# Performance work log

Hardware: AMD Instinct MI355X
Metric: run time of the kernel (lower is better)

## Reference

```python
import jax, jax.numpy as jnp
import numpy as np

B, D, E, TOP_K = 16384, 2048, 8, 2


def setup_inputs() -> dict:
    key = jax.random.key(0)
    ks = jax.random.split(key, 5)
    scale = 1.0 / np.sqrt(D)
    x = jax.random.normal(ks[0], (B, D), dtype=jnp.float32)
    # expert Linear(D, D) weights/biases, stacked over experts
    expert_w = jax.random.uniform(ks[1], (E, D, D), minval=-scale, maxval=scale, dtype=jnp.float32)
    expert_b = jax.random.uniform(ks[2], (E, D), minval=-scale, maxval=scale, dtype=jnp.float32)
    # gate Linear(D, E)
    gate_w = jax.random.uniform(ks[3], (D, E), minval=-scale, maxval=scale, dtype=jnp.float32)
    gate_b = jax.random.uniform(ks[4], (E,), minval=-scale, maxval=scale, dtype=jnp.float32)
    return {"x": x, "expert_w": expert_w, "expert_b": expert_b, "gate_w": gate_w, "gate_b": gate_b}


def reference(x, expert_w, expert_b, gate_w, gate_b):
    # gate logits: (B, E)
    logits = x @ gate_w + gate_b
    topk_logits, topk_idx = jax.lax.top_k(logits, TOP_K)          # (B, K)
    topk_weights = jax.nn.softmax(topk_logits, axis=-1)           # (B, K)
    # dense: compute every expert for every token (faithful to original)
    expert_outputs = jax.nn.relu(
        jnp.einsum("bd,edf->bef", x, expert_w) + expert_b[None, :, :]
    )                                                             # (B, E, D); dropout is identity in eval mode
    # gather the top-k experts per token
    selected = jnp.take_along_axis(expert_outputs, topk_idx[:, :, None], axis=1)  # (B, K, D)
    out = jnp.sum(selected * topk_weights[:, :, None], axis=1)    # (B, D)
    return out
```

## Files before the change

kernel.cpp:

```cpp
#include <hip/hip_runtime.h>
#include <hip/hip_bf16.h>
#include <math.h>

#define NB 16384
#define DD 2048
#define NE 8
#define TM 128
#define TN 128
#define BK 64
#define NKT (DD / BK)
#define MT_PER_PASS (NB / TM + NE)
#define NT_TILES (DD / TN)
#define GEMM_GRID (MT_PER_PASS * NT_TILES)

typedef float f32x4 __attribute__((ext_vector_type(4)));
typedef short bf16x8 __attribute__((ext_vector_type(8)));

__device__ __forceinline__ short f2bf(float f) {
  union { float f; unsigned u; } v; v.f = f;
  unsigned r = (v.u + 0x7FFFu + ((v.u >> 16) & 1u)) >> 16;
  return (short)r;
}

__device__ __forceinline__ void gload16(const void* g, void* l) {
  __builtin_amdgcn_global_load_lds((const __attribute__((address_space(1))) void*)g,
                                   (__attribute__((address_space(3))) void*)l,
                                   16, 0, 0);
}

__global__ void conv_wT(const float* __restrict__ w, short* __restrict__ wt) {
  __shared__ float tile[64][68];
  int bid = blockIdx.x;
  int e = bid >> 10;
  int tt = bid & 1023;
  int d0 = (tt >> 5) << 6;
  int f0 = (tt & 31) << 6;
  const float* we = w + (size_t)e * DD * DD;
  int t = threadIdx.x;
  int col = (t & 15) << 2;
#pragma unroll
  for (int p = 0; p < 4; ++p) {
    int dl = (t >> 4) + p * 16;
    f32x4 v = *(const f32x4*)(we + (size_t)(d0 + dl) * DD + f0 + col);
    *(f32x4*)&tile[dl][col] = v;
  }
  __syncthreads();
  int fl = t >> 2;
  int ds = (t & 3) << 4;
  short tmp[16];
#pragma unroll
  for (int j = 0; j < 16; ++j) tmp[j] = f2bf(tile[ds + j][fl]);
  short* dst = wt + (size_t)e * DD * DD + (size_t)(f0 + fl) * DD + d0 + ds;
  *(bf16x8*)dst = *(const bf16x8*)tmp;
  *(bf16x8*)(dst + 8) = *(const bf16x8*)(tmp + 8);
}

__global__ void gate_conv(const float* __restrict__ x, const float* __restrict__ gw,
                          const float* __restrict__ gb, short* __restrict__ xb,
                          int* __restrict__ ridx, float* __restrict__ rw) {
  int wid = threadIdx.x >> 6;
  int lane = threadIdx.x & 63;
  int b = blockIdx.x * 4 + wid;
  const float* xr = x + (size_t)b * DD;
  short* xbr = xb + (size_t)b * DD;
  double acc[8];
#pragma unroll
  for (int e = 0; e < 8; ++e) acc[e] = 0.0;
#pragma unroll
  for (int it = 0; it < 4; ++it) {
    int d8 = (it * 64 + lane) * 8;
    f32x4 a = *(const f32x4*)(xr + d8);
    f32x4 c = *(const f32x4*)(xr + d8 + 4);
    bf16x8 o;
    o[0] = f2bf(a[0]); o[1] = f2bf(a[1]); o[2] = f2bf(a[2]); o[3] = f2bf(a[3]);
    o[4] = f2bf(c[0]); o[5] = f2bf(c[1]); o[6] = f2bf(c[2]); o[7] = f2bf(c[3]);
    *(bf16x8*)(xbr + d8) = o;
#pragma unroll
    for (int j = 0; j < 8; ++j) {
      float xv = (j < 4) ? a[j] : c[j - 4];
      double xd = (double)xv;
      f32x4 g0 = *(const f32x4*)(gw + (size_t)(d8 + j) * 8);
      f32x4 g1 = *(const f32x4*)(gw + (size_t)(d8 + j) * 8 + 4);
      acc[0] += xd * g0[0]; acc[1] += xd * g0[1];
      acc[2] += xd * g0[2]; acc[3] += xd * g0[3];
      acc[4] += xd * g1[0]; acc[5] += xd * g1[1];
      acc[6] += xd * g1[2]; acc[7] += xd * g1[3];
    }
  }
#pragma unroll
  for (int off = 32; off > 0; off >>= 1) {
#pragma unroll
    for (int e = 0; e < 8; ++e) acc[e] += __shfl_down(acc[e], off);
  }
  if (lane == 0) {
    double l[8];
#pragma unroll
    for (int e = 0; e < 8; ++e) l[e] = acc[e] + (double)gb[e];
    int i0 = 0;
#pragma unroll
    for (int e = 1; e < 8; ++e) if (l[e] > l[i0]) i0 = e;
    int i1 = (i0 == 0) ? 1 : 0;
#pragma unroll
    for (int e = 0; e < 8; ++e) if (e != i0 && l[e] > l[i1]) i1 = e;
    double z = exp(l[i1] - l[i0]);
    float w0 = (float)(1.0 / (1.0 + z));
    float w1 = (float)(z / (1.0 + z));
    ridx[2 * b] = i0; ridx[2 * b + 1] = i1;
    rw[2 * b] = w0;   rw[2 * b + 1] = w1;
  }
}

__global__ void hist_tok(const int* __restrict__ ridx, int* __restrict__ partials) {
  __shared__ int h[16];
  int t = threadIdx.x;
  if (t < 16) h[t] = 0;
  __syncthreads();
  int t0 = blockIdx.x * 512;
  for (int i = t; i < 512; i += 256) {
    int tok = t0 + i;
    atomicAdd(&h[ridx[2 * tok]], 1);
    atomicAdd(&h[8 + ridx[2 * tok + 1]], 1);
  }
  __syncthreads();
  if (t < 16) partials[blockIdx.x * 16 + t] = h[t];
}

__global__ void scan_small(const int* __restrict__ partials, int* __restrict__ base,
                           int* __restrict__ cnts, int* __restrict__ offs) {
  __shared__ int c[16], o[16];
  int j = threadIdx.x;
  if (j < 16) {
    int s = 0;
    for (int b = 0; b < 32; ++b) s += partials[b * 16 + j];
    c[j] = s; cnts[j] = s;
  }
  __syncthreads();
  if (j < 2) {
    int a = 0;
    for (int e = 0; e < 8; ++e) { o[j * 8 + e] = a; a += c[j * 8 + e]; }
  }
  __syncthreads();
  if (j < 16) {
    int r = o[j];
    offs[j] = o[j];
    for (int b = 0; b < 32; ++b) { base[b * 16 + j] = r; r += partials[b * 16 + j]; }
  }
}

__global__ void scatter_tok(const int* __restrict__ ridx, const float* __restrict__ rw,
                            const int* __restrict__ base,
                            int* __restrict__ lists0, float* __restrict__ elw0,
                            int* __restrict__ lists1, float* __restrict__ elw1) {
  __shared__ int h[16];
  int t = threadIdx.x;
  if (t < 16) h[t] = 0;
  __syncthreads();
  int t0 = blockIdx.x * 512;
  const int* bb = base + blockIdx.x * 16;
  for (int i = t; i < 512; i += 256) {
    int tok = t0 + i;
    int e0 = ridx[2 * tok], e1 = ridx[2 * tok + 1];
    int r0 = atomicAdd(&h[e0], 1);
    int r1 = atomicAdd(&h[8 + e1], 1);
    int p0 = bb[e0] + r0;
    int p1 = bb[8 + e1] + r1;
    lists0[p0] = tok; elw0[p0] = rw[2 * tok];
    lists1[p1] = tok; elw1[p1] = rw[2 * tok + 1];
  }
}

template <int ADD>
__global__ __launch_bounds__(256, 4)
void moe_gemm(const short* __restrict__ xb, const short* __restrict__ wt,
              const float* __restrict__ eb, const int* __restrict__ cnts,
              const int* __restrict__ offs, const int* __restrict__ lists,
              const float* __restrict__ elw, float* __restrict__ out) {
  __shared__ short As[TM * BK];
  __shared__ short Bs[TN * BK];

  int bid = blockIdx.x;
  int xcd = bid & 7;
  int j = bid >> 3;
  int mt = xcd * 17 + (j >> 4);
  int nt = j & 15;

  int e = 0, cnt = 0;
  for (; e < NE; ++e) {
    cnt = cnts[e];
    int te = (cnt + TM - 1) >> 7;
    if (mt < te) break;
    mt -= te;
  }
  if (e >= NE) return;

  int m0 = mt * TM;
  int n0 = nt * TN;
  int off_e = offs[e];
  int tid = threadIdx.x;
  int lane = tid & 63, wid = tid >> 6;
  int wr = wid >> 1, wc = wid & 1;

  int trow = tid >> 3;
  int scol = ((tid & 7) ^ (trow & 7)) << 3;
  int tok[4];
#pragma unroll
  for (int l = 0; l < 4; ++l) {
    int gr = m0 + l * 32 + trow;
    tok[l] = lists[off_e + ((gr < cnt) ? gr : (cnt - 1))];
  }
  const short* bbase = wt + ((size_t)e * DD + (size_t)(n0 + trow)) * DD + scol;

  int lane15 = lane & 15;
  int csw0 = (((lane >> 4)    ) ^ (lane & 7)) << 3;
  int csw1 = (((lane >> 4) + 4) ^ (lane & 7)) << 3;
  int arow = (wr * 64 + lane15) * 64;
  int brow = (wc * 64 + lane15) * 64;

  f32x4 acc[4][4];
#pragma unroll
  for (int i = 0; i < 4; ++i)
#pragma unroll
    for (int j2 = 0; j2 < 4; ++j2) acc[i][j2] = (f32x4){0.f, 0.f, 0.f, 0.f};

#pragma unroll 1
  for (int kt = 0; kt < NKT; ++kt) {
    int ko = kt * BK + scol;
#pragma unroll
    for (int l = 0; l < 4; ++l) {
      gload16(xb + ((size_t)tok[l] << 11) + ko, &As[l * 2048 + tid * 8]);
      gload16(bbase + (size_t)(l * 32) * DD + kt * BK, &Bs[l * 2048 + tid * 8]);
    }
    __syncthreads();
    bf16x8 bfr[4][2];
#pragma unroll
    for (int j2 = 0; j2 < 4; ++j2) {
      int br = brow + j2 * 16 * 64;
      bfr[j2][0] = *(const bf16x8*)&Bs[br + csw0];
      bfr[j2][1] = *(const bf16x8*)&Bs[br + csw1];
    }
#pragma unroll
    for (int i = 0; i < 4; ++i) {
      int ar = arow + i * 16 * 64;
      bf16x8 a0 = *(const bf16x8*)&As[ar + csw0];
      bf16x8 a1 = *(const bf16x8*)&As[ar + csw1];
#pragma unroll
      for (int j2 = 0; j2 < 4; ++j2) {
        acc[i][j2] = __builtin_amdgcn_mfma_f32_16x16x32_bf16(a0, bfr[j2][0], acc[i][j2], 0, 0, 0);
        acc[i][j2] = __builtin_amdgcn_mfma_f32_16x16x32_bf16(a1, bfr[j2][1], acc[i][j2], 0, 0, 0);
      }
    }
    __syncthreads();
  }

  int r0 = (lane >> 4) << 2;
#pragma unroll
  for (int i = 0; i < 4; ++i) {
    int mloc = wr * 64 + i * 16 + r0;
#pragma unroll
    for (int r = 0; r < 4; ++r) {
      int gr = m0 + mloc + r;
      if (gr >= cnt) continue;
      int tokr = lists[off_e + gr];
      float wgt = elw[off_e + gr];
      float* orow = out + (size_t)tokr * DD;
#pragma unroll
      for (int j2 = 0; j2 < 4; ++j2) {
        int n = n0 + wc * 64 + j2 * 16 + lane15;
        float v = acc[i][j2][r] + eb[e * DD + n];
        v = fmaxf(v, 0.f) * wgt;
        if (ADD) v += __builtin_nontemporal_load(&orow[n]);
        __builtin_nontemporal_store(v, &orow[n]);
      }
    }
  }
}

extern "C" void kernel_launch(void* const* d_in, const int* in_sizes, int n_in,
                              void* d_out, int out_size, void* d_ws, size_t ws_size,
                              hipStream_t stream) {
  const float* x   = (const float*)d_in[0];
  const float* ewt = (const float*)d_in[1];
  const float* eb  = (const float*)d_in[2];
  const float* gw  = (const float*)d_in[3];
  const float* gb  = (const float*)d_in[4];
  float* out = (float*)d_out;

  char* ws = (char*)d_ws;
  short* xb      = (short*)(ws);
  short* wt      = (short*)(ws + 67108864);
  int*   ridx    = (int*)  (ws + 134217728);
  float* rw      = (float*)(ws + 134348800);
  int*   lists0  = (int*)  (ws + 134479872);
  float* elw0    = (float*)(ws + 134545408);
  int*   lists1  = (int*)  (ws + 134610944);
  float* elw1    = (float*)(ws + 134676480);
  int*   partials= (int*)  (ws + 134742016);
  int*   base    = (int*)  (ws + 134744064);
  int*   cnts    = (int*)  (ws + 134746112);
  int*   offs    = (int*)  (ws + 134746176);

  conv_wT<<<NE * 32 * 32, 256, 0, stream>>>(ewt, wt);
  gate_conv<<<NB / 4, 256, 0, stream>>>(x, gw, gb, xb, ridx, rw);
  hist_tok<<<32, 256, 0, stream>>>(ridx, partials);
  scan_small<<<1, 64, 0, stream>>>(partials, base, cnts, offs);
  scatter_tok<<<32, 256, 0, stream>>>(ridx, rw, base, lists0, elw0, lists1, elw1);
  moe_gemm<0><<<GEMM_GRID, 256, 0, stream>>>(xb, wt, eb, cnts,     offs,     lists0, elw0, out);
  moe_gemm<1><<<GEMM_GRID, 256, 0, stream>>>(xb, wt, eb, cnts + 8, offs + 8, lists1, elw1, out);
}
```

Measured before the change: 540.6 us.

## Merge weight conversion and gating into one kernel, replace histogram/scan with global atomics

```diff
diff --git a/kernel.cpp b/kernel.cpp
--- a/kernel.cpp
+++ b/kernel.cpp
@@ -12,6 +12,8 @@
 #define MT_PER_PASS (NB / TM + NE)
 #define NT_TILES (DD / TN)
 #define GEMM_GRID (MT_PER_PASS * NT_TILES)
+#define CONV_BLOCKS (NE * 32 * 32)
+#define GATE_BLOCKS (NB / 4)
 
 typedef float f32x4 __attribute__((ext_vector_type(4)));
 typedef short bf16x8 __attribute__((ext_vector_type(8)));
@@ -28,153 +30,120 @@
                                    16, 0, 0);
 }
 
-__global__ void conv_wT(const float* __restrict__ w, short* __restrict__ wt) {
+__global__ void prep(const float* __restrict__ w, short* __restrict__ wt,
+                     const float* __restrict__ x, const float* __restrict__ gw,
+                     const float* __restrict__ gb, short* __restrict__ xb,
+                     int* __restrict__ ridx, float* __restrict__ rw,
+                     int* __restrict__ cnts) {
   __shared__ float tile[64][68];
   int bid = blockIdx.x;
-  int e = bid >> 10;
-  int tt = bid & 1023;
-  int d0 = (tt >> 5) << 6;
-  int f0 = (tt & 31) << 6;
-  const float* we = w + (size_t)e * DD * DD;
   int t = threadIdx.x;
-  int col = (t & 15) << 2;
-#pragma unroll
-  for (int p = 0; p < 4; ++p) {
-    int dl = (t >> 4) + p * 16;
-    f32x4 v = *(const f32x4*)(we + (size_t)(d0 + dl) * DD + f0 + col);
-    *(f32x4*)&tile[dl][col] = v;
-  }
-  __syncthreads();
-  int fl = t >> 2;
-  int ds = (t & 3) << 4;
-  short tmp[16];
-#pragma unroll
-  for (int j = 0; j < 16; ++j) tmp[j] = f2bf(tile[ds + j][fl]);
-  short* dst = wt + (size_t)e * DD * DD + (size_t)(f0 + fl) * DD + d0 + ds;
-  *(bf16x8*)dst = *(const bf16x8*)tmp;
-  *(bf16x8*)(dst + 8) = *(const bf16x8*)(tmp + 8);
-}
-
-__global__ void gate_conv(const float* __restrict__ x, const float* __restrict__ gw,
-                          const float* __restrict__ gb, short* __restrict__ xb,
-                          int* __restrict__ ridx, float* __restrict__ rw) {
-  int wid = threadIdx.x >> 6;
-  int lane = threadIdx.x & 63;
-  int b = blockIdx.x * 4 + wid;
-  const float* xr = x + (size_t)b * DD;
-  short* xbr = xb + (size_t)b * DD;
-  double acc[8];
-#pragma unroll
-  for (int e = 0; e < 8; ++e) acc[e] = 0.0;
-#pragma unroll
-  for (int it = 0; it < 4; ++it) {
-    int d8 = (it * 64 + lane) * 8;
-    f32x4 a = *(const f32x4*)(xr + d8);
-    f32x4 c = *(const f32x4*)(xr + d8 + 4);
-    bf16x8 o;
-    o[0] = f2bf(a[0]); o[1] = f2bf(a[1]); o[2] = f2bf(a[2]); o[3] = f2bf(a[3]);
-    o[4] = f2bf(c[0]); o[5] = f2bf(c[1]); o[6] = f2bf(c[2]); o[7] = f2bf(c[3]);
-    *(bf16x8*)(xbr + d8) = o;
-#pragma unroll
-    for (int j = 0; j < 8; ++j) {
-      float xv = (j < 4) ? a[j] : c[j - 4];
-      double xd = (double)xv;
-      f32x4 g0 = *(const f32x4*)(gw + (size_t)(d8 + j) * 8);
-      f32x4 g1 = *(const f32x4*)(gw + (size_t)(d8 + j) * 8 + 4);
-      acc[0] += xd * g0[0]; acc[1] += xd * g0[1];
-      acc[2] += xd * g0[2]; acc[3] += xd * g0[3];
-      acc[4] += xd * g1[0]; acc[5] += xd * g1[1];
-      acc[6] += xd * g1[2]; acc[7] += xd * g1[3];
-    }
-  }
-#pragma unroll
-  for (int off = 32; off > 0; off >>= 1) {
-#pragma unroll
-    for (int e = 0; e < 8; ++e) acc[e] += __shfl_down(acc[e], off);
-  }
-  if (lane == 0) {
-    double l[8];
-#pragma unroll
-    for (int e = 0; e < 8; ++e) l[e] = acc[e] + (double)gb[e];
-    int i0 = 0;
-#pragma unroll
-    for (int e = 1; e < 8; ++e) if (l[e] > l[i0]) i0 = e;
-    int i1 = (i0 == 0) ? 1 : 0;
-#pragma unroll
-    for (int e = 0; e < 8; ++e) if (e != i0 && l[e] > l[i1]) i1 = e;
-    double z = exp(l[i1] - l[i0]);
-    float w0 = (float)(1.0 / (1.0 + z));
-    float w1 = (float)(z / (1.0 + z));
-    ridx[2 * b] = i0; ridx[2 * b + 1] = i1;
-    rw[2 * b] = w0;   rw[2 * b + 1] = w1;
-  }
-}
-
-__global__ void hist_tok(const int* __restrict__ ridx, int* __restrict__ partials) {
-  __shared__ int h[16];
-  int t = threadIdx.x;
-  if (t < 16) h[t] = 0;
-  __syncthreads();
-  int t0 = blockIdx.x * 512;
-  for (int i = t; i < 512; i += 256) {
-    int tok = t0 + i;
-    atomicAdd(&h[ridx[2 * tok]], 1);
-    atomicAdd(&h[8 + ridx[2 * tok + 1]], 1);
-  }
-  __syncthreads();
-  if (t < 16) partials[blockIdx.x * 16 + t] = h[t];
-}
-
-__global__ void scan_small(const int* __restrict__ partials, int* __restrict__ base,
-                           int* __restrict__ cnts, int* __restrict__ offs) {
-  __shared__ int c[16], o[16];
-  int j = threadIdx.x;
-  if (j < 16) {
-    int s = 0;
-    for (int b = 0; b < 32; ++b) s += partials[b * 16 + j];
-    c[j] = s; cnts[j] = s;
-  }
-  __syncthreads();
-  if (j < 2) {
-    int a = 0;
-    for (int e = 0; e < 8; ++e) { o[j * 8 + e] = a; a += c[j * 8 + e]; }
-  }
-  __syncthreads();
-  if (j < 16) {
-    int r = o[j];
-    offs[j] = o[j];
-    for (int b = 0; b < 32; ++b) { base[b * 16 + j] = r; r += partials[b * 16 + j]; }
+  if (bid < CONV_BLOCKS) {
+    int e = bid >> 10;
+    int tt = bid & 1023;
+    int d0 = (tt >> 5) << 6;
+    int f0 = (tt & 31) << 6;
+    const float* we = w + (size_t)e * DD * DD;
+    int col = (t & 15) << 2;
+#pragma unroll
+    for (int p = 0; p < 4; ++p) {
+      int dl = (t >> 4) + p * 16;
+      f32x4 v = *(const f32x4*)(we + (size_t)(d0 + dl) * DD + f0 + col);
+      *(f32x4*)&tile[dl][col] = v;
+    }
+    __syncthreads();
+    int fl = t >> 2;
+    int ds = (t & 3) << 4;
+    short tmp[16];
+#pragma unroll
+    for (int j = 0; j < 16; ++j) tmp[j] = f2bf(tile[ds + j][fl]);
+    short* dst = wt + (size_t)e * DD * DD + (size_t)(f0 + fl) * DD + d0 + ds;
+    *(bf16x8*)dst = *(const bf16x8*)tmp;
+    *(bf16x8*)(dst + 8) = *(const bf16x8*)(tmp + 8);
+  } else {
+    int wid = t >> 6;
+    int lane = t & 63;
+    int b = (bid - CONV_BLOCKS) * 4 + wid;
+    const float* xr = x + (size_t)b * DD;
+    short* xbr = xb + (size_t)b * DD;
+    double acc[8];
+#pragma unroll
+    for (int e = 0; e < 8; ++e) acc[e] = 0.0;
+#pragma unroll
+    for (int it = 0; it < 4; ++it) {
+      int d8 = (it * 64 + lane) * 8;
+      f32x4 a = *(const f32x4*)(xr + d8);
+      f32x4 c = *(const f32x4*)(xr + d8 + 4);
+      bf16x8 o;
+      o[0] = f2bf(a[0]); o[1] = f2bf(a[1]); o[2] = f2bf(a[2]); o[3] = f2bf(a[3]);
+      o[4] = f2bf(c[0]); o[5] = f2bf(c[1]); o[6] = f2bf(c[2]); o[7] = f2bf(c[3]);
+      *(bf16x8*)(xbr + d8) = o;
+#pragma unroll
+      for (int j = 0; j < 8; ++j) {
+        float xv = (j < 4) ? a[j] : c[j - 4];
+        double xd = (double)xv;
+        f32x4 g0 = *(const f32x4*)(gw + (size_t)(d8 + j) * 8);
+        f32x4 g1 = *(const f32x4*)(gw + (size_t)(d8 + j) * 8 + 4);
+        acc[0] += xd * g0[0]; acc[1] += xd * g0[1];
+        acc[2] += xd * g0[2]; acc[3] += xd * g0[3];
+        acc[4] += xd * g1[0]; acc[5] += xd * g1[1];
+        acc[6] += xd * g1[2]; acc[7] += xd * g1[3];
+      }
+    }
+#pragma unroll
+    for (int off = 32; off > 0; off >>= 1) {
+#pragma unroll
+      for (int e = 0; e < 8; ++e) acc[e] += __shfl_down(acc[e], off);
+    }
+    if (lane == 0) {
+      double l[8];
+#pragma unroll
+      for (int e = 0; e < 8; ++e) l[e] = acc[e] + (double)gb[e];
+      int i0 = 0;
+#pragma unroll
+      for (int e = 1; e < 8; ++e) if (l[e] > l[i0]) i0 = e;
+      int i1 = (i0 == 0) ? 1 : 0;
+#pragma unroll
+      for (int e = 0; e < 8; ++e) if (e != i0 && l[e] > l[i1]) i1 = e;
+      double z = exp(l[i1] - l[i0]);
+      float w0 = (float)(1.0 / (1.0 + z));
+      float w1 = (float)(z / (1.0 + z));
+      ridx[2 * b] = i0; ridx[2 * b + 1] = i1;
+      rw[2 * b] = w0;   rw[2 * b + 1] = w1;
+      atomicAdd(&cnts[i0], 1);
+      atomicAdd(&cnts[8 + i1], 1);
+    }
   }
 }
 
 __global__ void scatter_tok(const int* __restrict__ ridx, const float* __restrict__ rw,
-                            const int* __restrict__ base,
+                            const int* __restrict__ cnts, int* __restrict__ cursors,
                             int* __restrict__ lists0, float* __restrict__ elw0,
                             int* __restrict__ lists1, float* __restrict__ elw1) {
-  __shared__ int h[16];
+  __shared__ int offs[16];
   int t = threadIdx.x;
-  if (t < 16) h[t] = 0;
+  if (t < 2) {
+    int a = 0;
+#pragma unroll
+    for (int e = 0; e < 8; ++e) { offs[t * 8 + e] = a; a += cnts[t * 8 + e]; }
+  }
   __syncthreads();
-  int t0 = blockIdx.x * 512;
-  const int* bb = base + blockIdx.x * 16;
-  for (int i = t; i < 512; i += 256) {
-    int tok = t0 + i;
-    int e0 = ridx[2 * tok], e1 = ridx[2 * tok + 1];
-    int r0 = atomicAdd(&h[e0], 1);
-    int r1 = atomicAdd(&h[8 + e1], 1);
-    int p0 = bb[e0] + r0;
-    int p1 = bb[8 + e1] + r1;
-    lists0[p0] = tok; elw0[p0] = rw[2 * tok];
-    lists1[p1] = tok; elw1[p1] = rw[2 * tok + 1];
-  }
+  int tok = blockIdx.x * 256 + t;
+  int e0 = ridx[2 * tok], e1 = ridx[2 * tok + 1];
+  int r0 = atomicAdd(&cursors[e0], 1);
+  int r1 = atomicAdd(&cursors[8 + e1], 1);
+  int p0 = offs[e0] + r0;
+  int p1 = offs[8 + e1] + r1;
+  lists0[p0] = tok; elw0[p0] = rw[2 * tok];
+  lists1[p1] = tok; elw1[p1] = rw[2 * tok + 1];
 }
 
 template <int ADD>
 __global__ __launch_bounds__(256, 4)
 void moe_gemm(const short* __restrict__ xb, const short* __restrict__ wt,
               const float* __restrict__ eb, const int* __restrict__ cnts,
-              const int* __restrict__ offs, const int* __restrict__ lists,
-              const float* __restrict__ elw, float* __restrict__ out) {
+              const int* __restrict__ lists, const float* __restrict__ elw,
+              float* __restrict__ out) {
   __shared__ short As[TM * BK];
   __shared__ short Bs[TN * BK];
 
@@ -184,18 +153,18 @@
   int mt = xcd * 17 + (j >> 4);
   int nt = j & 15;
 
-  int e = 0, cnt = 0;
+  int e = 0, cnt = 0, off_e = 0;
   for (; e < NE; ++e) {
     cnt = cnts[e];
     int te = (cnt + TM - 1) >> 7;
     if (mt < te) break;
     mt -= te;
+    off_e += cnt;
   }
   if (e >= NE) return;
 
   int m0 = mt * TM;
   int n0 = nt * TN;
-  int off_e = offs[e];
   int tid = threadIdx.x;
   int lane = tid & 63, wid = tid >> 6;
   int wr = wid >> 1, wc = wid & 1;
@@ -294,16 +263,13 @@
   float* elw0    = (float*)(ws + 134545408);
   int*   lists1  = (int*)  (ws + 134610944);
   float* elw1    = (float*)(ws + 134676480);
-  int*   partials= (int*)  (ws + 134742016);
-  int*   base    = (int*)  (ws + 134744064);
-  int*   cnts    = (int*)  (ws + 134746112);
-  int*   offs    = (int*)  (ws + 134746176);
-
-  conv_wT<<<NE * 32 * 32, 256, 0, stream>>>(ewt, wt);
-  gate_conv<<<NB / 4, 256, 0, stream>>>(x, gw, gb, xb, ridx, rw);
-  hist_tok<<<32, 256, 0, stream>>>(ridx, partials);
-  scan_small<<<1, 64, 0, stream>>>(partials, base, cnts, offs);
-  scatter_tok<<<32, 256, 0, stream>>>(ridx, rw, base, lists0, elw0, lists1, elw1);
-  moe_gemm<0><<<GEMM_GRID, 256, 0, stream>>>(xb, wt, eb, cnts,     offs,     lists0, elw0, out);
-  moe_gemm<1><<<GEMM_GRID, 256, 0, stream>>>(xb, wt, eb, cnts + 8, offs + 8, lists1, elw1, out);
-}
+  int*   cnts    = (int*)  (ws + 134742016);
+  int*   cursors = (int*)  (ws + 134742080);
+
+  hipMemsetAsync(cnts, 0, 128, stream);
+
+  prep<<<CONV_BLOCKS + GATE_BLOCKS, 256, 0, stream>>>(ewt, wt, x, gw, gb, xb, ridx, rw, cnts);
+  scatter_tok<<<NB / 256, 256, 0, stream>>>(ridx, rw, cnts, cursors, lists0, elw0, lists1, elw1);
+  moe_gemm<0><<<GEMM_GRID, 256, 0, stream>>>(xb, wt, eb, cnts,     lists0, elw0, out);
+  moe_gemm<1><<<GEMM_GRID, 256, 0, stream>>>(xb, wt, eb, cnts + 8, lists1, elw1, out);
+}
```

Measured after the change: 907.1 us. 67.8% more time.
